# Kernel tuning notes

Hardware: AMD Instinct MI355X
Metric: run time of the kernel (lower is better)

The kernel has to match this reference:

```python
import jax, jax.numpy as jnp
import numpy as np

N_NODES = 50000
N_EDGES = 800000
NEG_SLOPE = 0.2


def gat_conv(x, W, al, ar, b, src, dst, num_nodes):
    # x: [N, Din]; W: [Din, H*Dout]; al/ar: [H, Dout]; b: [H*Dout]
    H, Dout = al.shape
    h = (x @ W).reshape(num_nodes, H, Dout)            # [N, H, Dout]
    el = jnp.sum(h * al[None], axis=-1)                # [N, H]
    er = jnp.sum(h * ar[None], axis=-1)                # [N, H]
    e = jax.nn.leaky_relu(el[src] + er[dst], NEG_SLOPE)  # [E, H]
    # segment softmax over incoming edges of each dst node
    m = jax.ops.segment_max(e, dst, num_segments=num_nodes)
    m = jnp.where(jnp.isfinite(m), m, 0.0)
    ex = jnp.exp(e - m[dst])                           # [E, H]
    s = jax.ops.segment_sum(ex, dst, num_segments=num_nodes)
    alpha = ex / s[dst]                                # [E, H]
    msg = h[src] * alpha[:, :, None]                   # [E, H, Dout]
    out = jax.ops.segment_sum(msg, dst, num_segments=num_nodes)
    return out + b.reshape(1, H, Dout)                 # [N, H, Dout]


def setup_inputs() -> dict:
    key = jax.random.key(0)
    ks = jax.random.split(key, 12)
    d_in, hid, heads = 128, 128, 2
    inp = {
        "embedding": jax.random.normal(ks[0], (N_NODES, d_in), jnp.float32),
        "W0": jax.random.normal(ks[1], (d_in, heads * hid), jnp.float32) * 0.1,
        "al0": jax.random.normal(ks[2], (heads, hid), jnp.float32) * 0.1,
        "ar0": jax.random.normal(ks[3], (heads, hid), jnp.float32) * 0.1,
        "b0": jnp.zeros((heads * hid,), jnp.float32),
        "W1": jax.random.normal(ks[4], (heads * hid, heads * hid), jnp.float32) * 0.1,
        "al1": jax.random.normal(ks[5], (1, heads * hid), jnp.float32) * 0.1,
        "ar1": jax.random.normal(ks[6], (1, heads * hid), jnp.float32) * 0.1,
        "b1": jnp.zeros((heads * hid,), jnp.float32),
        "src": jax.random.randint(ks[7], (N_EDGES,), 0, N_NODES, jnp.int32),
        "dst": jax.random.randint(ks[8], (N_EDGES,), 0, N_NODES, jnp.int32),
    }
    return inp


def reference(embedding, W0, al0, ar0, b0, W1, al1, ar1, b1, src, dst):
    n = embedding.shape[0]
    # layer 0: 2 heads, then flatten heads and ReLU (dropout no-op in eval)
    x = gat_conv(embedding, W0, al0, ar0, b0, src, dst, n)  # [N, 2, 128]
    x = jax.nn.relu(x.reshape(n, -1))                        # [N, 256]
    # layer 1: 1 head, squeeze
    x = gat_conv(x, W1, al1, ar1, b1, src, dst, n)           # [N, 1, 256]
    x = x.reshape(n, -1)
    x = x.at[0].set(0.0)
    return x
```

## Files before the change

kernel.cpp:

```cpp
#include <hip/hip_runtime.h>


typedef __attribute__((ext_vector_type(8))) short short8v;
typedef __attribute__((ext_vector_type(4))) float f32x4;

#define LOG2E 1.4426950408889634f

__device__ inline unsigned short f2bf(float x) {
    union { float f; unsigned int u; } v; v.f = x;
    unsigned int r = v.u + 0x7fffu + ((v.u >> 16) & 1u);
    return (unsigned short)(r >> 16);
}
__device__ inline float bf2f(unsigned short h) {
    union { unsigned int u; float f; } v; v.u = ((unsigned int)h) << 16;
    return v.f;
}

template<int AFP32, int H>
__global__ __launch_bounds__(256) void gemm_fused(
    const void* __restrict__ Av, const unsigned short* __restrict__ Bt,
    unsigned short* __restrict__ C,
    const float* __restrict__ al, const float* __restrict__ ar,
    float* __restrict__ el, float* __restrict__ er,
    int M, int N, int K)
{
    __shared__ __align__(16) unsigned short As[128 * 64];
    __shared__ __align__(16) unsigned short Bs[64 * 64];
    const int tid = threadIdx.x;
    const int lane = tid & 63, wv = tid >> 6;
    const int rowBase = blockIdx.x * 128;
    const int colBase = blockIdx.y * 64;

    f32x4 acc[2][4];
    #pragma unroll
    for (int i = 0; i < 2; ++i)
        #pragma unroll
        for (int j = 0; j < 4; ++j)
            acc[i][j] = (f32x4){0.f, 0.f, 0.f, 0.f};

    for (int k0 = 0; k0 < K; k0 += 64) {
        #pragma unroll
        for (int c = tid; c < 128 * 8; c += 256) {
            int row = c >> 3, cc = c & 7;
            int gr = rowBase + row; if (gr >= M) gr = M - 1;
            unsigned short* dstp = &As[row * 64 + (cc ^ (row & 7)) * 8];
            if (AFP32) {
                const float* A = (const float*)Av;
                const float* ap = A + (size_t)gr * K + k0 + cc * 8;
                float4 v0 = *(const float4*)ap;
                float4 v1 = *(const float4*)(ap + 4);
                ushort4 o0, o1;
                o0.x = f2bf(v0.x); o0.y = f2bf(v0.y); o0.z = f2bf(v0.z); o0.w = f2bf(v0.w);
                o1.x = f2bf(v1.x); o1.y = f2bf(v1.y); o1.z = f2bf(v1.z); o1.w = f2bf(v1.w);
                *(ushort4*)dstp = o0;
                *(ushort4*)(dstp + 4) = o1;
            } else {
                const unsigned short* A = (const unsigned short*)Av;
                int4 v = *(const int4*)(A + (size_t)gr * K + k0 + cc * 8);
                *(int4*)dstp = v;
            }
        }
        #pragma unroll
        for (int c = tid; c < 64 * 8; c += 256) {
            int n2 = c >> 3, cc = c & 7;
            int4 v = *(const int4*)(Bt + (size_t)(colBase + n2) * K + k0 + cc * 8);
            *(int4*)&Bs[n2 * 64 + (cc ^ (n2 & 7)) * 8] = v;
        }
        __syncthreads();

        #pragma unroll
        for (int ks = 0; ks < 64; ks += 32) {
            int kchunk = (ks >> 3) + (lane >> 4);
            short8v af[2], bfr[4];
            #pragma unroll
            for (int fm = 0; fm < 2; ++fm) {
                int ml = wv * 32 + fm * 16 + (lane & 15);
                af[fm] = *(const short8v*)&As[ml * 64 + (kchunk ^ (ml & 7)) * 8];
            }
            #pragma unroll
            for (int fi = 0; fi < 4; ++fi) {
                int nl = fi * 16 + (lane & 15);
                bfr[fi] = *(const short8v*)&Bs[nl * 64 + (kchunk ^ (nl & 7)) * 8];
            }
            #pragma unroll
            for (int fm = 0; fm < 2; ++fm)
                #pragma unroll
                for (int fi = 0; fi < 4; ++fi)
                    acc[fm][fi] = __builtin_amdgcn_mfma_f32_16x16x32_bf16(
                        af[fm], bfr[fi], acc[fm][fi], 0, 0, 0);
        }
        __syncthreads();
    }

    float alv[4], arv[4];
    #pragma unroll
    for (int fi = 0; fi < 4; ++fi) {
        int col = colBase + fi * 16 + (lane & 15);
        alv[fi] = al[col];
        arv[fi] = ar[col];
    }
    const int head = (H == 2) ? (colBase >> 7) : 0;

    #pragma unroll
    for (int fm = 0; fm < 2; ++fm) {
        #pragma unroll
        for (int r = 0; r < 4; ++r) {
            int row = rowBase + wv * 32 + fm * 16 + (lane >> 4) * 4 + r;
            float pe = acc[fm][0][r] * alv[0] + acc[fm][1][r] * alv[1]
                     + acc[fm][2][r] * alv[2] + acc[fm][3][r] * alv[3];
            float pr2 = acc[fm][0][r] * arv[0] + acc[fm][1][r] * arv[1]
                      + acc[fm][2][r] * arv[2] + acc[fm][3][r] * arv[3];
            #pragma unroll
            for (int off = 8; off; off >>= 1) {
                pe  += __shfl_xor(pe, off);
                pr2 += __shfl_xor(pr2, off);
            }
            if (row < M) {
                #pragma unroll
                for (int fi = 0; fi < 4; ++fi) {
                    int col = colBase + fi * 16 + (lane & 15);
                    C[(size_t)row * N + col] = f2bf(acc[fm][fi][r]);
                }
                if ((lane & 15) == 0) {
                    atomicAdd(&el[row * H + head], pe);
                    atomicAdd(&er[row * H + head], pr2);
                }
            }
        }
    }
}

__global__ void conv_count(const float* __restrict__ W0, unsigned short* __restrict__ W0t,
                           const float* __restrict__ W1, unsigned short* __restrict__ W1t,
                           const int* __restrict__ dst, int* __restrict__ cnt,
                           int nbW, int E)
{
    int bid = blockIdx.x;
    if (bid < nbW) {
        int t = bid * 256 + threadIdx.x;
        if (t < 128 * 256) {
            int k = t >> 8, n2 = t & 255;
            W0t[n2 * 128 + k] = f2bf(W0[t]);
        }
        int u = t - 128 * 256;
        if (u >= 0 && u < 256 * 256) {
            int k = u >> 8, n2 = u & 255;
            W1t[n2 * 256 + k] = f2bf(W1[u]);
        }
    } else {
        int t = (bid - nbW) * 256 + threadIdx.x;
        if (t < E) atomicAdd(&cnt[dst[t]], 1);
    }
}

__global__ __launch_bounds__(256) void scan_partial(const int* __restrict__ cnt,
                                                    int* __restrict__ bsum, int n)
{
    int t = threadIdx.x;
    int idx = blockIdx.x * 1024 + t * 4;
    int4 v = make_int4(0, 0, 0, 0);
    if (idx + 3 < n) v = *(const int4*)(cnt + idx);
    else if (idx < n) {
        v.x = cnt[idx];
        if (idx + 1 < n) v.y = cnt[idx + 1];
        if (idx + 2 < n) v.z = cnt[idx + 2];
    }
    int s = v.x + v.y + v.z + v.w;
    #pragma unroll
    for (int off = 32; off; off >>= 1) s += __shfl_xor(s, off);
    __shared__ int ws[4];
    if ((t & 63) == 0) ws[t >> 6] = s;
    __syncthreads();
    if (t == 0) bsum[blockIdx.x] = ws[0] + ws[1] + ws[2] + ws[3];
}

__global__ void scan_bsum(int* __restrict__ bsum, int* __restrict__ row,
                          int nb, int n, int E)
{
    int t = threadIdx.x;
    if (nb <= 64) {
        int v = (t < nb) ? bsum[t] : 0;
        int x = v;
        #pragma unroll
        for (int off = 1; off < 64; off <<= 1) {
            int y = __shfl_up(x, off);
            if (t >= off) x += y;
        }
        if (t < nb) bsum[t] = x - v;
    } else if (t == 0) {
        int run = 0;
        for (int i = 0; i < nb; ++i) { int v = bsum[i]; bsum[i] = run; run += v; }
    }
    if (t == 0) row[n] = E;
}

__global__ __launch_bounds__(256) void scan_final(
    const int* __restrict__ cnt, const int* __restrict__ bsum,
    int* __restrict__ row, int* __restrict__ cursor,
    float* __restrict__ el0, float* __restrict__ er0, int n)
{
    int t = threadIdx.x;
    int lane = t & 63;
    int idx = blockIdx.x * 1024 + t * 4;
    int4 v = make_int4(0, 0, 0, 0);
    if (idx + 3 < n) v = *(const int4*)(cnt + idx);
    else if (idx < n) {
        v.x = cnt[idx];
        if (idx + 1 < n) v.y = cnt[idx + 1];
        if (idx + 2 < n) v.z = cnt[idx + 2];
    }
    int s1 = v.x + v.y, s2 = s1 + v.z, s3 = s2 + v.w;
    int tsum = s3;
    int x = tsum;
    #pragma unroll
    for (int off = 1; off < 64; off <<= 1) {
        int y = __shfl_up(x, off);
        if (lane >= off) x += y;
    }
    int wex = x - tsum;
    __shared__ int ws[4];
    if (lane == 63) ws[t >> 6] = x;
    __syncthreads();
    int off0 = bsum[blockIdx.x];
    for (int w2 = 0; w2 < (t >> 6); ++w2) off0 += ws[w2];
    int e0 = off0 + wex;
    float2 z2 = make_float2(0.f, 0.f);
    if (idx < n)     { row[idx]     = e0;        cursor[idx]     = e0;
                       *(float2*)(el0 + 2*idx)     = z2; *(float2*)(er0 + 2*idx)     = z2; }
    if (idx + 1 < n) { row[idx + 1] = e0 + v.x;  cursor[idx + 1] = e0 + v.x;
                       *(float2*)(el0 + 2*idx + 2) = z2; *(float2*)(er0 + 2*idx + 2) = z2; }
    if (idx + 2 < n) { row[idx + 2] = e0 + s1;   cursor[idx + 2] = e0 + s1;
                       *(float2*)(el0 + 2*idx + 4) = z2; *(float2*)(er0 + 2*idx + 4) = z2; }
    if (idx + 3 < n) { row[idx + 3] = e0 + s2;   cursor[idx + 3] = e0 + s2;
                       *(float2*)(el0 + 2*idx + 6) = z2; *(float2*)(er0 + 2*idx + 6) = z2; }
}

__global__ void fill_kernel(const int* __restrict__ src, const int* __restrict__ dst,
                            int* __restrict__ cursor, int* __restrict__ srcc, int E)
{
    int t = blockIdx.x * blockDim.x + threadIdx.x;
    if (t < E) {
        int pos = atomicAdd(&cursor[dst[t]], 1);
        srcc[pos] = src[t];
    }
}

template<int H>
__global__ __launch_bounds__(256) void agg_kernel(
    const unsigned short* __restrict__ h, const float* __restrict__ el,
    const float* __restrict__ er, float* __restrict__ ecsr,
    const int* __restrict__ srcc, const int* __restrict__ row,
    const float* __restrict__ bias, float* __restrict__ outf,
    unsigned short* __restrict__ outb,
    float* __restrict__ elz, float* __restrict__ erz,
    int n_nodes, int E, int do_relu, int zero0)
{
    int wid = blockIdx.x * 4 + (threadIdx.x >> 6);
    if (wid >= n_nodes) return;
    int lane = threadIdx.x & 63;
    int beg = __builtin_amdgcn_readfirstlane(row[wid]);
    int end = __builtin_amdgcn_readfirstlane(row[wid + 1]);
    const int hsel   = (H == 2) ? (lane >> 5) : 0;
    const int stride = (H == 2) ? 32 : 64;
    const int l0     = (H == 2) ? (lane & 31) : lane;
    float* plane = ecsr + (size_t)hsel * E;
    const float rr = er[wid * H + hsel];

    if (elz && lane == 0) { elz[wid] = 0.f; erz[wid] = 0.f; }

    float m = -1e30f, s = 0.f;
    for (int i = beg + l0; i < end; i += stride) {
        int sn = srcc[i];
        float v = el[sn * H + hsel] + rr;
        float ev = ((v > 0.f) ? v : 0.2f * v) * LOG2E;
        plane[i] = ev;
        float mn = fmaxf(m, ev);
        s = s * exp2f(m - mn) + exp2f(ev - mn);
        m = mn;
    }
    #pragma unroll
    for (int off = (H == 2) ? 16 : 32; off; off >>= 1) {
        float mo = __shfl_xor(m, off);
        float so = __shfl_xor(s, off);
        float mn = fmaxf(m, mo);
        s = s * exp2f(m - mn) + so * exp2f(mo - mn);
        m = mn;
    }
    float r = (s > 0.f) ? 1.f / s : 0.f;
    __threadfence_block();

    float aA0 = 0.f, aA1 = 0.f, aA2 = 0.f, aA3 = 0.f;
    float aB0 = 0.f, aB1 = 0.f, aB2 = 0.f, aB3 = 0.f;
    float aC0 = 0.f, aC1 = 0.f, aC2 = 0.f, aC3 = 0.f;
    float aD0 = 0.f, aD1 = 0.f, aD2 = 0.f, aD3 = 0.f;
    int i = beg;
    for (; i + 3 < end; i += 4) {
        float wa = exp2f(plane[i]     - m);
        float wb = exp2f(plane[i + 1] - m);
        float wc = exp2f(plane[i + 2] - m);
        float wd = exp2f(plane[i + 3] - m);
        int sa = srcc[i], sb = srcc[i + 1], sc2 = srcc[i + 2], sd = srcc[i + 3];
        ushort4 ha = *(const ushort4*)(h + (size_t)sa * 256 + lane * 4);
        ushort4 hb = *(const ushort4*)(h + (size_t)sb * 256 + lane * 4);
        ushort4 hc = *(const ushort4*)(h + (size_t)sc2 * 256 + lane * 4);
        ushort4 hd = *(const ushort4*)(h + (size_t)sd * 256 + lane * 4);
        aA0 = fmaf(wa, bf2f(ha.x), aA0); aB0 = fmaf(wb, bf2f(hb.x), aB0);
        aC0 = fmaf(wc, bf2f(hc.x), aC0); aD0 = fmaf(wd, bf2f(hd.x), aD0);
        aA1 = fmaf(wa, bf2f(ha.y), aA1); aB1 = fmaf(wb, bf2f(hb.y), aB1);
        aC1 = fmaf(wc, bf2f(hc.y), aC1); aD1 = fmaf(wd, bf2f(hd.y), aD1);
        aA2 = fmaf(wa, bf2f(ha.z), aA2); aB2 = fmaf(wb, bf2f(hb.z), aB2);
        aC2 = fmaf(wc, bf2f(hc.z), aC2); aD2 = fmaf(wd, bf2f(hd.z), aD2);
        aA3 = fmaf(wa, bf2f(ha.w), aA3); aB3 = fmaf(wb, bf2f(hb.w), aB3);
        aC3 = fmaf(wc, bf2f(hc.w), aC3); aD3 = fmaf(wd, bf2f(hd.w), aD3);
    }
    for (; i < end; ++i) {
        float wa = exp2f(plane[i] - m);
        int sa = srcc[i];
        ushort4 ha = *(const ushort4*)(h + (size_t)sa * 256 + lane * 4);
        aA0 = fmaf(wa, bf2f(ha.x), aA0);
        aA1 = fmaf(wa, bf2f(ha.y), aA1);
        aA2 = fmaf(wa, bf2f(ha.z), aA2);
        aA3 = fmaf(wa, bf2f(ha.w), aA3);
    }

    float4 b4 = *(const float4*)(bias + lane * 4);
    float o0 = ((aA0 + aB0) + (aC0 + aD0)) * r + b4.x;
    float o1 = ((aA1 + aB1) + (aC1 + aD1)) * r + b4.y;
    float o2 = ((aA2 + aB2) + (aC2 + aD2)) * r + b4.z;
    float o3 = ((aA3 + aB3) + (aC3 + aD3)) * r + b4.w;
    if (do_relu) {
        o0 = fmaxf(o0, 0.f); o1 = fmaxf(o1, 0.f);
        o2 = fmaxf(o2, 0.f); o3 = fmaxf(o3, 0.f);
    }
    if (zero0 && wid == 0) { o0 = o1 = o2 = o3 = 0.f; }
    size_t base = (size_t)wid * 256 + lane * 4;
    if (outb) {
        ushort4 o; o.x = f2bf(o0); o.y = f2bf(o1); o.z = f2bf(o2); o.w = f2bf(o3);
        *(ushort4*)(outb + base) = o;
    } else {
        *(float4*)(outf + base) = make_float4(o0, o1, o2, o3);
    }
}

extern "C" void kernel_launch(void* const* d_in, const int* in_sizes, int n_in,
                              void* d_out, int out_size, void* d_ws, size_t ws_size,
                              hipStream_t stream)
{
    const float* emb = (const float*)d_in[0];
    const float* W0  = (const float*)d_in[1];
    const float* al0 = (const float*)d_in[2];
    const float* ar0 = (const float*)d_in[3];
    const float* b0  = (const float*)d_in[4];
    const float* W1  = (const float*)d_in[5];
    const float* al1 = (const float*)d_in[6];
    const float* ar1 = (const float*)d_in[7];
    const float* b1  = (const float*)d_in[8];
    const int* src   = (const int*)d_in[9];
    const int* dst   = (const int*)d_in[10];
    const int N = in_sizes[0] / 128;
    const int E = in_sizes[9];
    float* outp = (float*)d_out;

    char* w = (char*)d_ws;
    auto alloc = [&](size_t bytes) {
        char* p = w;
        w += (bytes + 255) & ~(size_t)255;
        return p;
    };
    unsigned short* hb  = (unsigned short*)alloc((size_t)N * 256 * 2);
    unsigned short* x1b = (unsigned short*)alloc((size_t)N * 256 * 2);
    float* ecsr = (float*)alloc((size_t)E * 2 * 4);
    int* srcc   = (int*)alloc((size_t)E * 4);
    int* rowp   = (int*)alloc((size_t)(N + 1) * 4);
    float* el0  = (float*)alloc((size_t)N * 2 * 4);
    float* er0  = (float*)alloc((size_t)N * 2 * 4);
    float* el1  = (float*)alloc((size_t)N * 4);
    float* er1  = (float*)alloc((size_t)N * 4);
    int* cnt    = (int*)alloc((size_t)N * 4);
    int* cursor = (int*)alloc((size_t)N * 4);
    int* bsum   = (int*)alloc(1024 * 4);
    unsigned short* W0t = (unsigned short*)alloc(256 * 128 * 2);
    unsigned short* W1t = (unsigned short*)alloc(256 * 256 * 2);

    const int nbScan = (N + 1023) / 1024;
    const int nbW = (128 * 256 + 256 * 256 + 255) / 256;

    hipMemsetAsync(cnt, 0, (size_t)N * 4, stream);
    conv_count<<<nbW + (E + 255) / 256, 256, 0, stream>>>(
        W0, W0t, W1, W1t, dst, cnt, nbW, E);
    scan_partial<<<nbScan, 256, 0, stream>>>(cnt, bsum, N);
    scan_bsum<<<1, 64, 0, stream>>>(bsum, rowp, nbScan, N, E);
    scan_final<<<nbScan, 256, 0, stream>>>(cnt, bsum, rowp, cursor, el0, er0, N);
    fill_kernel<<<(E + 255) / 256, 256, 0, stream>>>(src, dst, cursor, srcc, E);

    gemm_fused<1, 2><<<dim3((N + 127) / 128, 4), 256, 0, stream>>>(
        emb, W0t, hb, al0, ar0, el0, er0, N, 256, 128);
    agg_kernel<2><<<(N + 3) / 4, 256, 0, stream>>>(
        hb, el0, er0, ecsr, srcc, rowp, b0, nullptr, x1b, el1, er1, N, E, 1, 0);

    gemm_fused<0, 1><<<dim3((N + 127) / 128, 4), 256, 0, stream>>>(
        x1b, W1t, hb, al1, ar1, el1, er1, N, 256, 256);
    agg_kernel<1><<<(N + 3) / 4, 256, 0, stream>>>(
        hb, el1, er1, ecsr, srcc, rowp, b1, outp, nullptr, nullptr, nullptr, N, E, 0, 1);
}
```

Baseline: 291.6 us.

## Widen GEMM tile to 128 columns and pre-convert embedding to bf16

The GEMM column tile grows from 64 to 128, halving the grid's y dimension so each A tile is loaded and converted half as often, at the cost of more accumulator registers. The fp32-to-bf16 conversion of the embedding moves out of the layer-0 GEMM into a separate pass in the preprocessing kernel, written into the x1b buffer before it is needed. The GEMM template no longer needs an fp32 input path. Risks are lower occupancy from the larger accumulator set and an extra full read and write of the embedding.

Result: faster. 280.0 us (-4.0%).

```diff
diff --git a/kernel.cpp b/kernel.cpp
--- a/kernel.cpp
+++ b/kernel.cpp
@@ -16,26 +16,26 @@
     return v.f;
 }
 
-template<int AFP32, int H>
+template<int H>
 __global__ __launch_bounds__(256) void gemm_fused(
-    const void* __restrict__ Av, const unsigned short* __restrict__ Bt,
+    const unsigned short* __restrict__ A, const unsigned short* __restrict__ Bt,
     unsigned short* __restrict__ C,
     const float* __restrict__ al, const float* __restrict__ ar,
     float* __restrict__ el, float* __restrict__ er,
     int M, int N, int K)
 {
     __shared__ __align__(16) unsigned short As[128 * 64];
-    __shared__ __align__(16) unsigned short Bs[64 * 64];
+    __shared__ __align__(16) unsigned short Bs[128 * 64];
     const int tid = threadIdx.x;
     const int lane = tid & 63, wv = tid >> 6;
     const int rowBase = blockIdx.x * 128;
-    const int colBase = blockIdx.y * 64;
-
-    f32x4 acc[2][4];
+    const int colBase = blockIdx.y * 128;
+
+    f32x4 acc[2][8];
     #pragma unroll
     for (int i = 0; i < 2; ++i)
         #pragma unroll
-        for (int j = 0; j < 4; ++j)
+        for (int j = 0; j < 8; ++j)
             acc[i][j] = (f32x4){0.f, 0.f, 0.f, 0.f};
 
     for (int k0 = 0; k0 < K; k0 += 64) {
@@ -43,25 +43,11 @@
         for (int c = tid; c < 128 * 8; c += 256) {
             int row = c >> 3, cc = c & 7;
             int gr = rowBase + row; if (gr >= M) gr = M - 1;
-            unsigned short* dstp = &As[row * 64 + (cc ^ (row & 7)) * 8];
-            if (AFP32) {
-                const float* A = (const float*)Av;
-                const float* ap = A + (size_t)gr * K + k0 + cc * 8;
-                float4 v0 = *(const float4*)ap;
-                float4 v1 = *(const float4*)(ap + 4);
-                ushort4 o0, o1;
-                o0.x = f2bf(v0.x); o0.y = f2bf(v0.y); o0.z = f2bf(v0.z); o0.w = f2bf(v0.w);
-                o1.x = f2bf(v1.x); o1.y = f2bf(v1.y); o1.z = f2bf(v1.z); o1.w = f2bf(v1.w);
-                *(ushort4*)dstp = o0;
-                *(ushort4*)(dstp + 4) = o1;
-            } else {
-                const unsigned short* A = (const unsigned short*)Av;
-                int4 v = *(const int4*)(A + (size_t)gr * K + k0 + cc * 8);
-                *(int4*)dstp = v;
-            }
-        }
-        #pragma unroll
-        for (int c = tid; c < 64 * 8; c += 256) {
+            int4 v = *(const int4*)(A + (size_t)gr * K + k0 + cc * 8);
+            *(int4*)&As[row * 64 + (cc ^ (row & 7)) * 8] = v;
+        }
+        #pragma unroll
+        for (int c = tid; c < 128 * 8; c += 256) {
             int n2 = c >> 3, cc = c & 7;
             int4 v = *(const int4*)(Bt + (size_t)(colBase + n2) * K + k0 + cc * 8);
             *(int4*)&Bs[n2 * 64 + (cc ^ (n2 & 7)) * 8] = v;
@@ -71,30 +57,30 @@
         #pragma unroll
         for (int ks = 0; ks < 64; ks += 32) {
             int kchunk = (ks >> 3) + (lane >> 4);
-            short8v af[2], bfr[4];
+            short8v af[2], bfr[8];
             #pragma unroll
             for (int fm = 0; fm < 2; ++fm) {
                 int ml = wv * 32 + fm * 16 + (lane & 15);
                 af[fm] = *(const short8v*)&As[ml * 64 + (kchunk ^ (ml & 7)) * 8];
             }
             #pragma unroll
-            for (int fi = 0; fi < 4; ++fi) {
+            for (int fi = 0; fi < 8; ++fi) {
                 int nl = fi * 16 + (lane & 15);
                 bfr[fi] = *(const short8v*)&Bs[nl * 64 + (kchunk ^ (nl & 7)) * 8];
             }
             #pragma unroll
             for (int fm = 0; fm < 2; ++fm)
                 #pragma unroll
-                for (int fi = 0; fi < 4; ++fi)
+                for (int fi = 0; fi < 8; ++fi)
                     acc[fm][fi] = __builtin_amdgcn_mfma_f32_16x16x32_bf16(
                         af[fm], bfr[fi], acc[fm][fi], 0, 0, 0);
         }
         __syncthreads();
     }
 
-    float alv[4], arv[4];
-    #pragma unroll
-    for (int fi = 0; fi < 4; ++fi) {
+    float alv[8], arv[8];
+    #pragma unroll
+    for (int fi = 0; fi < 8; ++fi) {
         int col = colBase + fi * 16 + (lane & 15);
         alv[fi] = al[col];
         arv[fi] = ar[col];
@@ -106,10 +92,12 @@
         #pragma unroll
         for (int r = 0; r < 4; ++r) {
             int row = rowBase + wv * 32 + fm * 16 + (lane >> 4) * 4 + r;
-            float pe = acc[fm][0][r] * alv[0] + acc[fm][1][r] * alv[1]
-                     + acc[fm][2][r] * alv[2] + acc[fm][3][r] * alv[3];
-            float pr2 = acc[fm][0][r] * arv[0] + acc[fm][1][r] * arv[1]
-                      + acc[fm][2][r] * arv[2] + acc[fm][3][r] * arv[3];
+            float pe = 0.f, pr2 = 0.f;
+            #pragma unroll
+            for (int fi = 0; fi < 8; ++fi) {
+                pe  = fmaf(acc[fm][fi][r], alv[fi], pe);
+                pr2 = fmaf(acc[fm][fi][r], arv[fi], pr2);
+            }
             #pragma unroll
             for (int off = 8; off; off >>= 1) {
                 pe  += __shfl_xor(pe, off);
@@ -117,7 +105,7 @@
             }
             if (row < M) {
                 #pragma unroll
-                for (int fi = 0; fi < 4; ++fi) {
+                for (int fi = 0; fi < 8; ++fi) {
                     int col = colBase + fi * 16 + (lane & 15);
                     C[(size_t)row * N + col] = f2bf(acc[fm][fi][r]);
                 }
@@ -132,8 +120,9 @@
 
 __global__ void conv_count(const float* __restrict__ W0, unsigned short* __restrict__ W0t,
                            const float* __restrict__ W1, unsigned short* __restrict__ W1t,
+                           const float* __restrict__ emb, unsigned short* __restrict__ embb,
                            const int* __restrict__ dst, int* __restrict__ cnt,
-                           int nbW, int E)
+                           int nbW, int nbE, int E, int nEmb)
 {
     int bid = blockIdx.x;
     if (bid < nbW) {
@@ -147,9 +136,17 @@
             int k = u >> 8, n2 = u & 255;
             W1t[n2 * 256 + k] = f2bf(W1[u]);
         }
-    } else {
+    } else if (bid < nbW + nbE) {
         int t = (bid - nbW) * 256 + threadIdx.x;
         if (t < E) atomicAdd(&cnt[dst[t]], 1);
+    } else {
+        int t = ((bid - nbW - nbE) * 256 + threadIdx.x) * 4;
+        if (t + 3 < nEmb) {
+            float4 v = *(const float4*)(emb + t);
+            ushort4 o;
+            o.x = f2bf(v.x); o.y = f2bf(v.y); o.z = f2bf(v.z); o.w = f2bf(v.w);
+            *(ushort4*)(embb + t) = o;
+        }
     }
 }
 
@@ -369,6 +366,7 @@
     };
     unsigned short* hb  = (unsigned short*)alloc((size_t)N * 256 * 2);
     unsigned short* x1b = (unsigned short*)alloc((size_t)N * 256 * 2);
+    unsigned short* embb = x1b;
     float* ecsr = (float*)alloc((size_t)E * 2 * 4);
     int* srcc   = (int*)alloc((size_t)E * 4);
     int* rowp   = (int*)alloc((size_t)(N + 1) * 4);
@@ -384,21 +382,24 @@
 
     const int nbScan = (N + 1023) / 1024;
     const int nbW = (128 * 256 + 256 * 256 + 255) / 256;
+    const int nbE = (E + 255) / 256;
+    const int nEmb = N * 128;
+    const int nbEmb = (nEmb / 4 + 255) / 256;
 
     hipMemsetAsync(cnt, 0, (size_t)N * 4, stream);
-    conv_count<<<nbW + (E + 255) / 256, 256, 0, stream>>>(
-        W0, W0t, W1, W1t, dst, cnt, nbW, E);
+    conv_count<<<nbW + nbE + nbEmb, 256, 0, stream>>>(
+        W0, W0t, W1, W1t, emb, embb, dst, cnt, nbW, nbE, E, nEmb);
     scan_partial<<<nbScan, 256, 0, stream>>>(cnt, bsum, N);
     scan_bsum<<<1, 64, 0, stream>>>(bsum, rowp, nbScan, N, E);
     scan_final<<<nbScan, 256, 0, stream>>>(cnt, bsum, rowp, cursor, el0, er0, N);
-    fill_kernel<<<(E + 255) / 256, 256, 0, stream>>>(src, dst, cursor, srcc, E);
-
-    gemm_fused<1, 2><<<dim3((N + 127) / 128, 4), 256, 0, stream>>>(
-        emb, W0t, hb, al0, ar0, el0, er0, N, 256, 128);
+    fill_kernel<<<nbE, 256, 0, stream>>>(src, dst, cursor, srcc, E);
+
+    gemm_fused<2><<<dim3((N + 127) / 128, 2), 256, 0, stream>>>(
+        embb, W0t, hb, al0, ar0, el0, er0, N, 256, 128);
     agg_kernel<2><<<(N + 3) / 4, 256, 0, stream>>>(
         hb, el0, er0, ecsr, srcc, rowp, b0, nullptr, x1b, el1, er1, N, E, 1, 0);
 
-    gemm_fused<0, 1><<<dim3((N + 127) / 128, 4), 256, 0, stream>>>(
+    gemm_fused<1><<<dim3((N + 127) / 128, 2), 256, 0, stream>>>(
         x1b, W1t, hb, al1, ar1, el1, er1, N, 256, 256);
     agg_kernel<1><<<(N + 3) / 4, 256, 0, stream>>>(
         hb, el1, er1, ecsr, srcc, rowp, b1, outp, nullptr, nullptr, nullptr, N, E, 0, 1);
```
